# Kernel tuning notes

Measured on AMD Instinct MI355X. Metric: run time of the kernel, lower is better.

Reference implementation:

```python
import jax, jax.numpy as jnp
import numpy as np

NEG_INF = -1000000.0  # same fill value as the torch module


def setup_inputs() -> dict:
    key = jax.random.key(0)
    kq, kk, kv, kl = jax.random.split(key, 4)
    B, S, D = 32, 2048, 64
    queries = jax.random.normal(kq, (B, S, D), dtype=jnp.float32)
    keys = jax.random.normal(kk, (B, S, D), dtype=jnp.float32)
    values = jax.random.normal(kv, (B, S, D), dtype=jnp.float32)
    valid_lens = jax.random.randint(kl, (B,), 0, 2048, dtype=jnp.int32)
    return {"queries": queries, "keys": keys, "values": values, "valid_lens": valid_lens}


def reference(queries, keys, values, valid_lens):
    d = queries.shape[-1]
    # scores: [B, Sq, Sk]
    scores = jnp.einsum("bqd,bkd->bqk", queries, keys) / jnp.sqrt(jnp.asarray(d, queries.dtype))
    # mask key positions >= valid_len (valid_lens is per-batch, broadcast over queries)
    kpos = jnp.arange(scores.shape[-1])
    mask = kpos[None, None, :] < valid_lens[:, None, None]
    scores = jnp.where(mask, scores, jnp.asarray(NEG_INF, scores.dtype))
    attention_weights = jax.nn.softmax(scores, axis=-1)
    output = jnp.einsum("bqk,bkd->bqd", attention_weights, values)
    return output, attention_weights
```

## Files before the change

kernel.cpp:

```cpp
#include <hip/hip_runtime.h>
#include <hip/hip_bf16.h>
#include <math.h>


constexpr int BB = 32;
constexpr int SS = 2048;
constexpr int DD = 64;

typedef float  f32x4  __attribute__((ext_vector_type(4)));
typedef __bf16 b16x8  __attribute__((ext_vector_type(8)));

static __device__ __forceinline__ f32x4 mfma16(b16x8 a, b16x8 b, f32x4 c) {
    return __builtin_amdgcn_mfma_f32_16x16x32_bf16(a, b, c, 0, 0, 0);
}

static __device__ __forceinline__ void stage64x64(const float* __restrict__ g,
                                                  __bf16* __restrict__ s, int t) {
    const int row = t >> 2, c0 = (t & 3) * 16;
    const float4* gp = (const float4*)(g + row * 64 + c0);
    float4 f0 = gp[0], f1 = gp[1], f2 = gp[2], f3 = gp[3];
    float v[16] = {f0.x, f0.y, f0.z, f0.w, f1.x, f1.y, f1.z, f1.w,
                   f2.x, f2.y, f2.z, f2.w, f3.x, f3.y, f3.z, f3.w};
    const int base = ((row >> 4) * 2 + (c0 >> 5)) * 512 +
                     (((c0 >> 3) & 3) * 16 + (row & 15)) * 8;
    b16x8 a, b;
#pragma unroll
    for (int i = 0; i < 8; ++i) { a[i] = (__bf16)v[i]; b[i] = (__bf16)v[8 + i]; }
    *(b16x8*)&s[base]       = a;
    *(b16x8*)&s[base + 128] = b;
}

static __device__ __forceinline__ void stageV64x64(const float* __restrict__ g,
                                                   __bf16* __restrict__ s, int t) {
    const int key = t >> 2, c0 = (t & 3) * 16;
    const float4* gp = (const float4*)(g + key * 64 + c0);
    float4 f0 = gp[0], f1 = gp[1], f2 = gp[2], f3 = gp[3];
    float v[16] = {f0.x, f0.y, f0.z, f0.w, f1.x, f1.y, f1.z, f1.w,
                   f2.x, f2.y, f2.z, f2.w, f3.x, f3.y, f3.z, f3.w};
    const int base = ((c0 >> 4) * 2 + (key >> 5)) * 512 +
                     (((key >> 3) & 3) * 16) * 8 + (key & 7);
#pragma unroll
    for (int i = 0; i < 16; ++i) s[base + i * 8] = (__bf16)v[i];
}

__global__ __launch_bounds__(256)
void attn_o_kernel(const float* __restrict__ Q, const float* __restrict__ K,
                   const float* __restrict__ V, const int* __restrict__ VL,
                   float* __restrict__ O, float* __restrict__ W)
{
    __shared__ __align__(16) __bf16 Qs[4096], Ks[4096], Vs[4096];
    __shared__ __align__(16) __bf16 Ps[4][1024];

    const int t = threadIdx.x, lane = t & 63, wave = t >> 6;
    const int quad = lane >> 4, lq = lane & 15;
    const int b = blockIdx.x >> 5, qg = blockIdx.x & 31;

    const int  L    = VL[b];
    const bool uni  = (L == 0);
    const int  Leff = uni ? SS : L;
    const int  ntiles = (Leff + 63) >> 6;

    stage64x64(Q + ((size_t)b * SS + qg * 64) * DD, Qs, t);
    __syncthreads();

    const b16x8 aq0 = *(const b16x8*)&Qs[(wave * 2 + 0) * 512 + lane * 8];
    const b16x8 aq1 = *(const b16x8*)&Qs[(wave * 2 + 1) * 512 + lane * 8];

    f32x4 o[4];
#pragma unroll
    for (int d = 0; d < 4; ++d) o[d] = (f32x4){0.f, 0.f, 0.f, 0.f};
    float lp[4] = {0.f, 0.f, 0.f, 0.f};

    for (int kt = 0; kt < ntiles; ++kt) {
        const int kb = kt * 64;
        __syncthreads();
        stage64x64 (K + ((size_t)b * SS + kb) * DD, Ks, t);
        stageV64x64(V + ((size_t)b * SS + kb) * DD, Vs, t);
        __syncthreads();

#pragma unroll
        for (int ct = 0; ct < 4; ++ct) {
            f32x4 c = (f32x4){0.f, 0.f, 0.f, 0.f};
            c = mfma16(aq0, *(const b16x8*)&Ks[(ct * 2 + 0) * 512 + lane * 8], c);
            c = mfma16(aq1, *(const b16x8*)&Ks[(ct * 2 + 1) * 512 + lane * 8], c);
            const int key = kb + ct * 16 + lq;
#pragma unroll
            for (int r = 0; r < 4; ++r) {
                float w = uni ? 1.0f : __expf(c[r] * 0.125f);
                w = (key < Leff) ? w : 0.0f;
                lp[r] += w;
                Ps[wave][(ct >> 1) * 512 +
                         (((ct * 2 + (lq >> 3)) & 3) * 16 + quad * 4 + r) * 8 +
                         (lq & 7)] = (__bf16)w;
            }
        }
        __syncthreads();

        const b16x8 ap0 = *(const b16x8*)&Ps[wave][0   + lane * 8];
        const b16x8 ap1 = *(const b16x8*)&Ps[wave][512 + lane * 8];
#pragma unroll
        for (int ds = 0; ds < 4; ++ds) {
            o[ds] = mfma16(ap0, *(const b16x8*)&Vs[(ds * 2 + 0) * 512 + lane * 8], o[ds]);
            o[ds] = mfma16(ap1, *(const b16x8*)&Vs[(ds * 2 + 1) * 512 + lane * 8], o[ds]);
        }
    }

    float inv[4];
#pragma unroll
    for (int r = 0; r < 4; ++r) {
        float l = lp[r];
        l += __shfl_xor(l, 1); l += __shfl_xor(l, 2);
        l += __shfl_xor(l, 4); l += __shfl_xor(l, 8);
        inv[r] = 1.0f / l;
    }

    const int qrow = qg * 64 + wave * 16 + quad * 4;
#pragma unroll
    for (int ds = 0; ds < 4; ++ds)
#pragma unroll
        for (int r = 0; r < 4; ++r)
            O[((size_t)b * SS + qrow + r) * DD + ds * 16 + lq] = o[ds][r] * inv[r];

    if (lq == 0) {
#pragma unroll
        for (int r = 0; r < 4; ++r)
            W[((size_t)b * SS + qrow + r) * SS + (SS - 1)] = inv[r];
    }
}

__global__ __launch_bounds__(256)
void attn_w_kernel(const float* __restrict__ Q, const float* __restrict__ K,
                   const int* __restrict__ VL, float* __restrict__ W)
{
    __shared__ __align__(16) __bf16 Qs[4096], Ks[4096];

    const int t = threadIdx.x, lane = t & 63, wave = t >> 6;
    const int quad = lane >> 4, lq = lane & 15;
    const int b = blockIdx.x >> 5, qg = blockIdx.x & 31;

    const int  L   = VL[b];
    const bool uni = (L == 0);
    const int  ntiles = uni ? 0 : (L + 63) >> 6;
    const int  kfill  = ntiles * 64;
    const float fillv = uni ? (1.0f / 2048.0f) : 0.0f;
    const int  qrow = qg * 64 + wave * 16 + quad * 4;

    float inv[4] = {0.f, 0.f, 0.f, 0.f};
    if (!uni) {
#pragma unroll
        for (int r = 0; r < 4; ++r)
            inv[r] = W[((size_t)b * SS + qrow + r) * SS + (SS - 1)];
    }

    stage64x64(Q + ((size_t)b * SS + qg * 64) * DD, Qs, t);
    __syncthreads();

    const b16x8 aq0 = *(const b16x8*)&Qs[(wave * 2 + 0) * 512 + lane * 8];
    const b16x8 aq1 = *(const b16x8*)&Qs[(wave * 2 + 1) * 512 + lane * 8];

    for (int kt = 0; kt < ntiles; ++kt) {
        const int kb = kt * 64;
        __syncthreads();
        stage64x64(K + ((size_t)b * SS + kb) * DD, Ks, t);
        __syncthreads();

#pragma unroll
        for (int ct = 0; ct < 4; ++ct) {
            f32x4 c = (f32x4){0.f, 0.f, 0.f, 0.f};
            c = mfma16(aq0, *(const b16x8*)&Ks[(ct * 2 + 0) * 512 + lane * 8], c);
            c = mfma16(aq1, *(const b16x8*)&Ks[(ct * 2 + 1) * 512 + lane * 8], c);
            const int key = kb + ct * 16 + lq;
#pragma unroll
            for (int r = 0; r < 4; ++r) {
                float w = __expf(c[r] * 0.125f) * inv[r];
                w = (key < L) ? w : 0.0f;
                W[((size_t)b * SS + qrow + r) * SS + key] = w;
            }
        }
    }

    for (int row = 0; row < 64; ++row) {
        float* base = W + ((size_t)b * SS + qg * 64 + row) * SS;
        for (int c = kfill + t * 4; c < SS; c += 1024)
            *(float4*)(base + c) = make_float4(fillv, fillv, fillv, fillv);
    }
}

extern "C" void kernel_launch(void* const* d_in, const int* in_sizes, int n_in,
                              void* d_out, int out_size, void* d_ws, size_t ws_size,
                              hipStream_t stream) {
    const float* Q  = (const float*)d_in[0];
    const float* K  = (const float*)d_in[1];
    const float* V  = (const float*)d_in[2];
    const int*   VL = (const int*)d_in[3];
    float* O = (float*)d_out;
    float* W = (float*)d_out + (size_t)BB * SS * DD;

    dim3 grid(BB * (SS / 64)), block(256);
    attn_o_kernel<<<grid, block, 0, stream>>>(Q, K, V, VL, O, W);
    attn_w_kernel<<<grid, block, 0, stream>>>(Q, K, VL, W);
}
```

Measured before the change: 726.6 us.

## Pre-convert Q/K/V to bf16 tiles and fuse attention kernels with async LDS loads

```diff
diff --git a/kernel.cpp b/kernel.cpp
--- a/kernel.cpp
+++ b/kernel.cpp
@@ -12,6 +12,12 @@
 
 static __device__ __forceinline__ f32x4 mfma16(b16x8 a, b16x8 b, f32x4 c) {
     return __builtin_amdgcn_mfma_f32_16x16x32_bf16(a, b, c, 0, 0, 0);
+}
+
+static __device__ __forceinline__ void gload16(const __bf16* g, __bf16* l) {
+    __builtin_amdgcn_global_load_lds(
+        (const __attribute__((address_space(1))) unsigned int*)(const void*)g,
+        (__attribute__((address_space(3))) unsigned int*)(void*)l, 16, 0, 0);
 }
 
 static __device__ __forceinline__ void stage64x64(const float* __restrict__ g,
@@ -44,6 +50,161 @@
 }
 
 __global__ __launch_bounds__(256)
+void convert_kernel(const float* __restrict__ Q, const float* __restrict__ K,
+                    const float* __restrict__ V,
+                    __bf16* __restrict__ Qb, __bf16* __restrict__ Kb,
+                    __bf16* __restrict__ Vb)
+{
+    __shared__ __align__(16) __bf16 tmp[4096];
+    const int t = threadIdx.x;
+    const size_t blk = blockIdx.x;
+    const size_t goff = blk * 4096;
+
+    stage64x64(Q + goff, tmp, t);
+    __syncthreads();
+    { b16x8 a = *(const b16x8*)&tmp[t * 8], b = *(const b16x8*)&tmp[2048 + t * 8];
+      *(b16x8*)(Qb + goff + t * 8) = a; *(b16x8*)(Qb + goff + 2048 + t * 8) = b; }
+    __syncthreads();
+
+    stage64x64(K + goff, tmp, t);
+    __syncthreads();
+    { b16x8 a = *(const b16x8*)&tmp[t * 8], b = *(const b16x8*)&tmp[2048 + t * 8];
+      *(b16x8*)(Kb + goff + t * 8) = a; *(b16x8*)(Kb + goff + 2048 + t * 8) = b; }
+    __syncthreads();
+
+    stageV64x64(V + goff, tmp, t);
+    __syncthreads();
+    { b16x8 a = *(const b16x8*)&tmp[t * 8], b = *(const b16x8*)&tmp[2048 + t * 8];
+      *(b16x8*)(Vb + goff + t * 8) = a; *(b16x8*)(Vb + goff + 2048 + t * 8) = b; }
+}
+
+__global__ __launch_bounds__(256)
+void attn_fused(const __bf16* __restrict__ Qb, const __bf16* __restrict__ Kb,
+                const __bf16* __restrict__ Vb, const int* __restrict__ VL,
+                float* __restrict__ O, float* __restrict__ W)
+{
+    __shared__ __align__(16) __bf16 Ks[2][4096], Vs[2][4096];
+    __shared__ __align__(16) __bf16 Ps[4][1024];
+
+    const int t = threadIdx.x, lane = t & 63, wave = t >> 6;
+    const int quad = lane >> 4, lq = lane & 15;
+    const int swz = (blockIdx.x & 7) * 128 + (blockIdx.x >> 3);
+    const int b = swz >> 5, qg = swz & 31;
+
+    const int  L    = VL[b];
+    const bool uni  = (L == 0);
+    const int  Leff = uni ? SS : L;
+    const int  ntiles = (Leff + 63) >> 6;
+
+    const __bf16* qt = Qb + (size_t)swz * 4096;
+    const b16x8 aq0 = *(const b16x8*)(qt + (wave * 2 + 0) * 512 + lane * 8);
+    const b16x8 aq1 = *(const b16x8*)(qt + (wave * 2 + 1) * 512 + lane * 8);
+
+    const __bf16* kbase = Kb + (size_t)b * 32 * 4096;
+    const __bf16* vbase = Vb + (size_t)b * 32 * 4096;
+
+    auto stageK = [&](int kt, int s) {
+        const __bf16* src = kbase + (size_t)kt * 4096;
+        gload16(src + wave * 512 + lane * 8,        &Ks[s][wave * 512]);
+        gload16(src + 2048 + wave * 512 + lane * 8, &Ks[s][2048 + wave * 512]);
+    };
+    auto stageV = [&](int kt, int s) {
+        const __bf16* src = vbase + (size_t)kt * 4096;
+        gload16(src + wave * 512 + lane * 8,        &Vs[s][wave * 512]);
+        gload16(src + 2048 + wave * 512 + lane * 8, &Vs[s][2048 + wave * 512]);
+    };
+
+    f32x4 o[4];
+#pragma unroll
+    for (int d = 0; d < 4; ++d) o[d] = (f32x4){0.f, 0.f, 0.f, 0.f};
+    float lp[4] = {0.f, 0.f, 0.f, 0.f};
+
+    int buf = 0;
+    stageK(0, 0); stageV(0, 0);
+    __syncthreads();
+
+    for (int kt = 0; kt < ntiles; ++kt) {
+        if (kt + 1 < ntiles) { stageK(kt + 1, buf ^ 1); stageV(kt + 1, buf ^ 1); }
+
+#pragma unroll
+        for (int ct = 0; ct < 4; ++ct) {
+            f32x4 c = (f32x4){0.f, 0.f, 0.f, 0.f};
+            c = mfma16(aq0, *(const b16x8*)&Ks[buf][(ct * 2 + 0) * 512 + lane * 8], c);
+            c = mfma16(aq1, *(const b16x8*)&Ks[buf][(ct * 2 + 1) * 512 + lane * 8], c);
+            const int key = kt * 64 + ct * 16 + lq;
+#pragma unroll
+            for (int r = 0; r < 4; ++r) {
+                float w = uni ? 1.0f : __expf(c[r] * 0.125f);
+                w = (key < Leff) ? w : 0.0f;
+                lp[r] += w;
+                Ps[wave][(ct >> 1) * 512 +
+                         (((ct * 2 + (lq >> 3)) & 3) * 16 + quad * 4 + r) * 8 +
+                         (lq & 7)] = (__bf16)w;
+            }
+        }
+        const b16x8 ap0 = *(const b16x8*)&Ps[wave][0   + lane * 8];
+        const b16x8 ap1 = *(const b16x8*)&Ps[wave][512 + lane * 8];
+#pragma unroll
+        for (int ds = 0; ds < 4; ++ds) {
+            o[ds] = mfma16(ap0, *(const b16x8*)&Vs[buf][(ds * 2 + 0) * 512 + lane * 8], o[ds]);
+            o[ds] = mfma16(ap1, *(const b16x8*)&Vs[buf][(ds * 2 + 1) * 512 + lane * 8], o[ds]);
+        }
+        __syncthreads();
+        buf ^= 1;
+    }
+
+    float inv[4];
+#pragma unroll
+    for (int r = 0; r < 4; ++r) {
+        float l = lp[r];
+        l += __shfl_xor(l, 1); l += __shfl_xor(l, 2);
+        l += __shfl_xor(l, 4); l += __shfl_xor(l, 8);
+        inv[r] = 1.0f / l;
+    }
+
+    const int qrow = qg * 64 + wave * 16 + quad * 4;
+#pragma unroll
+    for (int ds = 0; ds < 4; ++ds)
+#pragma unroll
+        for (int r = 0; r < 4; ++r)
+            O[((size_t)b * SS + qrow + r) * DD + ds * 16 + lq] = o[ds][r] * inv[r];
+
+    const int  nt2   = uni ? 0 : ntiles;
+    const int  kfill = nt2 * 64;
+    const float fillv = uni ? (1.0f / 2048.0f) : 0.0f;
+
+    if (nt2 > 0) {
+        buf = 0;
+        stageK(0, 0);
+        __syncthreads();
+        for (int kt = 0; kt < nt2; ++kt) {
+            if (kt + 1 < nt2) stageK(kt + 1, buf ^ 1);
+#pragma unroll
+            for (int ct = 0; ct < 4; ++ct) {
+                f32x4 c = (f32x4){0.f, 0.f, 0.f, 0.f};
+                c = mfma16(aq0, *(const b16x8*)&Ks[buf][(ct * 2 + 0) * 512 + lane * 8], c);
+                c = mfma16(aq1, *(const b16x8*)&Ks[buf][(ct * 2 + 1) * 512 + lane * 8], c);
+                const int key = kt * 64 + ct * 16 + lq;
+#pragma unroll
+                for (int r = 0; r < 4; ++r) {
+                    float w = __expf(c[r] * 0.125f) * inv[r];
+                    w = (key < L) ? w : 0.0f;
+                    W[((size_t)b * SS + qrow + r) * SS + key] = w;
+                }
+            }
+            __syncthreads();
+            buf ^= 1;
+        }
+    }
+
+    for (int row = 0; row < 64; ++row) {
+        float* base = W + ((size_t)b * SS + qg * 64 + row) * SS;
+        for (int c = kfill + t * 4; c < SS; c += 1024)
+            *(float4*)(base + c) = make_float4(fillv, fillv, fillv, fillv);
+    }
+}
+
+__global__ __launch_bounds__(256)
 void attn_o_kernel(const float* __restrict__ Q, const float* __restrict__ K,
                    const float* __restrict__ V, const int* __restrict__ VL,
                    float* __restrict__ O, float* __restrict__ W)
@@ -196,7 +357,19 @@
     float* O = (float*)d_out;
     float* W = (float*)d_out + (size_t)BB * SS * DD;
 
-    dim3 grid(BB * (SS / 64)), block(256);
-    attn_o_kernel<<<grid, block, 0, stream>>>(Q, K, V, VL, O, W);
-    attn_w_kernel<<<grid, block, 0, stream>>>(Q, K, VL, W);
-}
+    const size_t nElem = (size_t)BB * SS * DD;
+    const size_t need  = nElem * 2 * 3;
+
+    if (d_ws != nullptr && ws_size >= need) {
+        __bf16* Qb = (__bf16*)d_ws;
+        __bf16* Kb = Qb + nElem;
+        __bf16* Vb = Kb + nElem;
+        dim3 grid(BB * (SS / 64)), block(256);
+        convert_kernel<<<grid, block, 0, stream>>>(Q, K, V, Qb, Kb, Vb);
+        attn_fused<<<grid, block, 0, stream>>>(Qb, Kb, Vb, VL, O, W);
+    } else {
+        dim3 grid(BB * (SS / 64)), block(256);
+        attn_o_kernel<<<grid, block, 0, stream>>>(Q, K, V, VL, O, W);
+        attn_w_kernel<<<grid, block, 0, stream>>>(Q, K, VL, W);
+    }
+}
```

Measured after the change: 647.4 us. -10.9%, faster.
